# Optimization experiments

Measured on AMD Instinct MI355X. Metric: run time of the kernel, lower is better.

## Reference

```python
import jax, jax.numpy as jnp
import numpy as np

B = 1048576   # batch
D = 128       # input_dim
S = 4         # num_quantum_states


def setup_inputs() -> dict:
    key = jax.random.key(0)
    ks = jax.random.split(key, 7)
    x = jax.random.normal(ks[0], (B, D), dtype=jnp.float32)
    # fused per-state Linear(input_dim, 1) weights -> [D, S] matrix + [S] bias
    W = jax.random.normal(ks[1], (D, S), dtype=jnp.float32) * (1.0 / np.sqrt(D))
    b = jax.random.normal(ks[2], (S,), dtype=jnp.float32) * 0.1
    # interference matrix: randn*0.1 + I
    M = jax.random.normal(ks[3], (S, S), dtype=jnp.float32) * 0.1 + jnp.eye(S, dtype=jnp.float32)
    threshold = jnp.float32(0.5)
    noise = jax.random.normal(ks[4], (B, 1), dtype=jnp.float32)       # torch.randn(batch,1)
    u = jax.random.uniform(ks[5], (B, 1), dtype=jnp.float32)          # bernoulli draw
    ug = jax.random.uniform(ks[6], (B, S), dtype=jnp.float32, minval=1e-7, maxval=1.0 - 1e-7)
    gumbel = -jnp.log(-jnp.log(ug))                                   # multinomial draw
    return {"x": x, "W": W, "b": b, "M": M, "threshold": threshold,
            "noise": noise, "u": u, "gumbel": gumbel}


def reference(x, W, b, M, threshold, noise, u, gumbel):
    # per-state sigmoid(Linear(x)) fused: [B, S]
    state_tensor = jax.nn.sigmoid(x @ W + b)
    # interference: state_tensor @ M.T -> [B, S]
    interfered = state_tensor @ M.T
    # measurement probability and bernoulli collapse decision
    measurement_prob = jax.nn.sigmoid(noise + threshold)              # [B, 1]
    should_measure = u < measurement_prob                             # bool [B, 1]
    # multinomial over softmax(interfered[b]) == argmax(logits + gumbel)
    chosen = jnp.argmax(interfered + gumbel, axis=-1, keepdims=True)  # [B, 1]
    measured_val = jnp.take_along_axis(interfered, chosen, axis=-1)   # [B, 1]
    superposition_output = jnp.mean(interfered, axis=-1, keepdims=True)
    collapsed_output = jnp.where(should_measure, measured_val, superposition_output)
    return collapsed_output
```

## Files before the change

### kernel.cpp

```cpp
#include <hip/hip_runtime.h>
#include <math.h>

__global__ __launch_bounds__(256) void superpos_kernel(
    const float4* __restrict__ x4,
    const float4* __restrict__ W4,
    const float*  __restrict__ bvec,
    const float*  __restrict__ M,
    const float*  __restrict__ thrp,
    const float*  __restrict__ noise,
    const float*  __restrict__ u,
    const float4* __restrict__ gum4,
    float*        __restrict__ out,
    int B)
{
    const int tid = threadIdx.x;
    const int s   = tid & 7;
    const int row = blockIdx.x * 32 + (tid >> 3);
    if (row >= B) return;

    const float4* __restrict__ xrow = x4 + (size_t)row * 32;

    float d0 = 0.f, d1 = 0.f, d2 = 0.f, d3 = 0.f;
    #pragma unroll
    for (int j = 0; j < 4; ++j) {
        const int c = s + 8 * j;
        const float4 xv = xrow[c];
        const float4 w0 = W4[c * 4 + 0];
        const float4 w1 = W4[c * 4 + 1];
        const float4 w2 = W4[c * 4 + 2];
        const float4 w3 = W4[c * 4 + 3];
        d0 += xv.x * w0.x + xv.y * w1.x + xv.z * w2.x + xv.w * w3.x;
        d1 += xv.x * w0.y + xv.y * w1.y + xv.z * w2.y + xv.w * w3.y;
        d2 += xv.x * w0.z + xv.y * w1.z + xv.z * w2.z + xv.w * w3.z;
        d3 += xv.x * w0.w + xv.y * w1.w + xv.z * w2.w + xv.w * w3.w;
    }

    #pragma unroll
    for (int off = 4; off >= 1; off >>= 1) {
        d0 += __shfl_xor(d0, off, 8);
        d1 += __shfl_xor(d1, off, 8);
        d2 += __shfl_xor(d2, off, 8);
        d3 += __shfl_xor(d3, off, 8);
    }

    const float st0 = 1.0f / (1.0f + expf(-(d0 + bvec[0])));
    const float st1 = 1.0f / (1.0f + expf(-(d1 + bvec[1])));
    const float st2 = 1.0f / (1.0f + expf(-(d2 + bvec[2])));
    const float st3 = 1.0f / (1.0f + expf(-(d3 + bvec[3])));

    const float i0 = st0*M[ 0] + st1*M[ 1] + st2*M[ 2] + st3*M[ 3];
    const float i1 = st0*M[ 4] + st1*M[ 5] + st2*M[ 6] + st3*M[ 7];
    const float i2 = st0*M[ 8] + st1*M[ 9] + st2*M[10] + st3*M[11];
    const float i3 = st0*M[12] + st1*M[13] + st2*M[14] + st3*M[15];

    const float prob   = 1.0f / (1.0f + expf(-(noise[row] + thrp[0])));
    const bool  should = u[row] < prob;

    const float4 g = gum4[row];
    float best = i0 + g.x; int ch = 0;
    float v;
    v = i1 + g.y; if (v > best) { best = v; ch = 1; }
    v = i2 + g.z; if (v > best) { best = v; ch = 2; }
    v = i3 + g.w; if (v > best) { best = v; ch = 3; }
    const float meas = (ch == 0) ? i0 : (ch == 1) ? i1 : (ch == 2) ? i2 : i3;

    const float mean = 0.25f * (i0 + i1 + i2 + i3);
    const float result = should ? meas : mean;

    if (s == 0) out[row] = result;
}

extern "C" void kernel_launch(void* const* d_in, const int* in_sizes, int n_in,
                              void* d_out, int out_size, void* d_ws, size_t ws_size,
                              hipStream_t stream) {
    const float4* x4    = (const float4*)d_in[0];
    const float4* W4    = (const float4*)d_in[1];
    const float*  bvec  = (const float*)d_in[2];
    const float*  M     = (const float*)d_in[3];
    const float*  thrp  = (const float*)d_in[4];
    const float*  noise = (const float*)d_in[5];
    const float*  u     = (const float*)d_in[6];
    const float4* gum4  = (const float4*)d_in[7];
    float*        out   = (float*)d_out;

    const int B = out_size;
    const int grid = (B + 31) / 32;
    superpos_kernel<<<grid, 256, 0, stream>>>(x4, W4, bvec, M, thrp, noise, u,
                                              gum4, out, B);
}
```

Measured before the change: 718.7 us.

## Process four rows per 8-lane group to reuse W loads and vectorize I/O

Each group of 8 lanes now handles four consecutive rows, so the W float4 loads are reused across four rows of x. The per-row noise and u values are loaded as float4, and the four results are written with a single float4 store. The grid shrinks fourfold. This trades more registers and fewer resident waves for less redundant W traffic and fewer small memory transactions. The x reads per lane are now strided by a full row, and the code assumes B is a multiple of 4.

```diff
diff --git a/kernel.cpp b/kernel.cpp
--- a/kernel.cpp
+++ b/kernel.cpp
@@ -10,64 +10,89 @@
     const float*  __restrict__ noise,
     const float*  __restrict__ u,
     const float4* __restrict__ gum4,
-    float*        __restrict__ out,
+    float4*       __restrict__ out4,
     int B)
 {
     const int tid = threadIdx.x;
     const int s   = tid & 7;
-    const int row = blockIdx.x * 32 + (tid >> 3);
-    if (row >= B) return;
+    const int g   = tid >> 3;
+    const int rbase = blockIdx.x * 128 + g * 4;
+    if (rbase >= B) return;
 
-    const float4* __restrict__ xrow = x4 + (size_t)row * 32;
+    const float4* __restrict__ x0 = x4 + (size_t)rbase * 32;
 
-    float d0 = 0.f, d1 = 0.f, d2 = 0.f, d3 = 0.f;
+    float d[4][4];
+    #pragma unroll
+    for (int rr = 0; rr < 4; ++rr) {
+        d[rr][0] = 0.f; d[rr][1] = 0.f; d[rr][2] = 0.f; d[rr][3] = 0.f;
+    }
+
     #pragma unroll
     for (int j = 0; j < 4; ++j) {
         const int c = s + 8 * j;
-        const float4 xv = xrow[c];
         const float4 w0 = W4[c * 4 + 0];
         const float4 w1 = W4[c * 4 + 1];
         const float4 w2 = W4[c * 4 + 2];
         const float4 w3 = W4[c * 4 + 3];
-        d0 += xv.x * w0.x + xv.y * w1.x + xv.z * w2.x + xv.w * w3.x;
-        d1 += xv.x * w0.y + xv.y * w1.y + xv.z * w2.y + xv.w * w3.y;
-        d2 += xv.x * w0.z + xv.y * w1.z + xv.z * w2.z + xv.w * w3.z;
-        d3 += xv.x * w0.w + xv.y * w1.w + xv.z * w2.w + xv.w * w3.w;
+        #pragma unroll
+        for (int rr = 0; rr < 4; ++rr) {
+            const float4 xv = x0[rr * 32 + c];
+            d[rr][0] += xv.x * w0.x + xv.y * w1.x + xv.z * w2.x + xv.w * w3.x;
+            d[rr][1] += xv.x * w0.y + xv.y * w1.y + xv.z * w2.y + xv.w * w3.y;
+            d[rr][2] += xv.x * w0.z + xv.y * w1.z + xv.z * w2.z + xv.w * w3.z;
+            d[rr][3] += xv.x * w0.w + xv.y * w1.w + xv.z * w2.w + xv.w * w3.w;
+        }
     }
 
     #pragma unroll
-    for (int off = 4; off >= 1; off >>= 1) {
-        d0 += __shfl_xor(d0, off, 8);
-        d1 += __shfl_xor(d1, off, 8);
-        d2 += __shfl_xor(d2, off, 8);
-        d3 += __shfl_xor(d3, off, 8);
+    for (int rr = 0; rr < 4; ++rr) {
+        #pragma unroll
+        for (int off = 4; off >= 1; off >>= 1) {
+            d[rr][0] += __shfl_xor(d[rr][0], off, 8);
+            d[rr][1] += __shfl_xor(d[rr][1], off, 8);
+            d[rr][2] += __shfl_xor(d[rr][2], off, 8);
+            d[rr][3] += __shfl_xor(d[rr][3], off, 8);
+        }
     }
 
-    const float st0 = 1.0f / (1.0f + expf(-(d0 + bvec[0])));
-    const float st1 = 1.0f / (1.0f + expf(-(d1 + bvec[1])));
-    const float st2 = 1.0f / (1.0f + expf(-(d2 + bvec[2])));
-    const float st3 = 1.0f / (1.0f + expf(-(d3 + bvec[3])));
+    const float b0 = bvec[0], b1 = bvec[1], b2 = bvec[2], b3 = bvec[3];
+    const float thr = thrp[0];
+    const float4 n4  = *reinterpret_cast<const float4*>(noise + rbase);
+    const float4 uv4 = *reinterpret_cast<const float4*>(u + rbase);
 
-    const float i0 = st0*M[ 0] + st1*M[ 1] + st2*M[ 2] + st3*M[ 3];
-    const float i1 = st0*M[ 4] + st1*M[ 5] + st2*M[ 6] + st3*M[ 7];
-    const float i2 = st0*M[ 8] + st1*M[ 9] + st2*M[10] + st3*M[11];
-    const float i3 = st0*M[12] + st1*M[13] + st2*M[14] + st3*M[15];
+    float res[4];
+    #pragma unroll
+    for (int rr = 0; rr < 4; ++rr) {
+        const float st0 = 1.0f / (1.0f + expf(-(d[rr][0] + b0)));
+        const float st1 = 1.0f / (1.0f + expf(-(d[rr][1] + b1)));
+        const float st2 = 1.0f / (1.0f + expf(-(d[rr][2] + b2)));
+        const float st3 = 1.0f / (1.0f + expf(-(d[rr][3] + b3)));
 
-    const float prob   = 1.0f / (1.0f + expf(-(noise[row] + thrp[0])));
-    const bool  should = u[row] < prob;
+        const float i0 = st0*M[ 0] + st1*M[ 1] + st2*M[ 2] + st3*M[ 3];
+        const float i1 = st0*M[ 4] + st1*M[ 5] + st2*M[ 6] + st3*M[ 7];
+        const float i2 = st0*M[ 8] + st1*M[ 9] + st2*M[10] + st3*M[11];
+        const float i3 = st0*M[12] + st1*M[13] + st2*M[14] + st3*M[15];
 
-    const float4 g = gum4[row];
-    float best = i0 + g.x; int ch = 0;
-    float v;
-    v = i1 + g.y; if (v > best) { best = v; ch = 1; }
-    v = i2 + g.z; if (v > best) { best = v; ch = 2; }
-    v = i3 + g.w; if (v > best) { best = v; ch = 3; }
-    const float meas = (ch == 0) ? i0 : (ch == 1) ? i1 : (ch == 2) ? i2 : i3;
+        const float nse = (rr == 0) ? n4.x : (rr == 1) ? n4.y : (rr == 2) ? n4.z : n4.w;
+        const float uvv = (rr == 0) ? uv4.x : (rr == 1) ? uv4.y : (rr == 2) ? uv4.z : uv4.w;
+        const float prob   = 1.0f / (1.0f + expf(-(nse + thr)));
+        const bool  should = uvv < prob;
 
-    const float mean = 0.25f * (i0 + i1 + i2 + i3);
-    const float result = should ? meas : mean;
+        const float4 gv = gum4[rbase + rr];
+        float best = i0 + gv.x; int ch = 0;
+        float v;
+        v = i1 + gv.y; if (v > best) { best = v; ch = 1; }
+        v = i2 + gv.z; if (v > best) { best = v; ch = 2; }
+        v = i3 + gv.w; if (v > best) { best = v; ch = 3; }
+        const float meas = (ch == 0) ? i0 : (ch == 1) ? i1 : (ch == 2) ? i2 : i3;
 
-    if (s == 0) out[row] = result;
+        const float mean = 0.25f * (i0 + i1 + i2 + i3);
+        res[rr] = should ? meas : mean;
+    }
+
+    if (s == 0) {
+        out4[rbase >> 2] = make_float4(res[0], res[1], res[2], res[3]);
+    }
 }
 
 extern "C" void kernel_launch(void* const* d_in, const int* in_sizes, int n_in,
@@ -81,10 +106,10 @@
     const float*  noise = (const float*)d_in[5];
     const float*  u     = (const float*)d_in[6];
     const float4* gum4  = (const float4*)d_in[7];
-    float*        out   = (float*)d_out;
+    float4*       out4  = (float4*)d_out;
 
     const int B = out_size;
-    const int grid = (B + 31) / 32;
+    const int grid = (B + 127) / 128;
     superpos_kernel<<<grid, 256, 0, stream>>>(x4, W4, bvec, M, thrp, noise, u,
-                                              gum4, out, B);
+                                              gum4, out4, B);
 }
```

Result: faster. 698.5 us (-2.8%).
